# Kernel optimization log

Hardware: AMD Instinct MI355X
Metric: run time of the kernel (lower is better)

The kernel has to match this reference:

```python
import jax, jax.numpy as jnp
import numpy as np

B, T, D, U = 32, 2048, 512, 512


def setup_inputs() -> dict:
    key = jax.random.key(0)
    ks = jax.random.split(key, 6)
    scale = 0.05
    return {
        "values": jax.random.normal(ks[0], (B, T, D), dtype=jnp.float32),
        "query": jax.random.normal(ks[1], (B, D), dtype=jnp.float32),
        "W1_w": jax.random.normal(ks[2], (D, U), dtype=jnp.float32) * scale,
        "W1_b": jnp.zeros((U,), dtype=jnp.float32),
        "W2_w": jax.random.normal(ks[3], (D, U), dtype=jnp.float32) * scale,
        "W2_b": jnp.zeros((U,), dtype=jnp.float32),
        "V_w": jax.random.normal(ks[4], (U, 1), dtype=jnp.float32) * scale,
        "V_b": jnp.zeros((1,), dtype=jnp.float32),
    }


def reference(values, query, W1_w, W1_b, W2_w, W2_b, V_w, V_b):
    # values: [B, T, D]; query: [B, D]
    proj_v = jnp.einsum("btd,du->btu", values, W1_w) + W1_b          # [B, T, U]
    proj_q = (query @ W2_w + W2_b)[:, None, :]                        # [B, 1, U]
    score = jnp.tanh(proj_v + proj_q) @ V_w + V_b                     # [B, T, 1]
    attention_weights = jax.nn.softmax(score, axis=1)                 # [B, T, 1]
    context_vector = jnp.sum(attention_weights * values, axis=1)      # [B, D]
    return context_vector, attention_weights
```

## Files before the change

### kernel.cpp

```cpp
#include <hip/hip_runtime.h>
#include <hip/hip_bf16.h>
#include <stdint.h>


#define B_DIM 32
#define T_DIM 2048
#define D_DIM 512
#define U_DIM 512
#define M_DIM (B_DIM * T_DIM)

typedef short bf16x8 __attribute__((ext_vector_type(8)));
typedef float f32x4 __attribute__((ext_vector_type(4)));

__device__ __forceinline__ float fast_tanh(float x) {
    float e = __expf(2.0f * x);
    return 1.0f - __fdividef(2.0f, e + 1.0f);
}

__device__ __forceinline__ short bf16r(float x) {
    unsigned u = __float_as_uint(x);
    u += 0x7fffu + ((u >> 16) & 1u);
    return (short)(u >> 16);
}


__global__ void prep_kernel(const float* __restrict__ W1_w,
                            const float* __restrict__ W1_b,
                            const float* __restrict__ W2_w,
                            const float* __restrict__ W2_b,
                            const float* __restrict__ query,
                            unsigned short* __restrict__ W1T,
                            float* __restrict__ qb) {
    __shared__ float red[256];
    const int tid = threadIdx.x;
    if (blockIdx.x < 128) {
        int n = blockIdx.x * 256 + tid;
        int uu    = n & 255;
        int kc    = (n >> 8) & 3;
        int kstep = (n >> 10) & 15;
        int ut    = n >> 14;
        int u  = ut * 256 + uu;
        int k0 = kstep * 32 + kc * 8;
        bf16x8 pk;
#pragma unroll
        for (int j = 0; j < 8; ++j)
            pk[j] = bf16r(W1_w[(size_t)(k0 + j) * U_DIM + u]);
        ((bf16x8*)W1T)[n] = pk;
    } else {
        int bid = blockIdx.x - 128;
        int b  = bid >> 3;
        int ug = bid & 7;
        int u  = ug * 64 + (tid & 63);
        int dq = tid >> 6;
        const float* q  = query + b * D_DIM + dq * 128;
        const float* w2 = W2_w + (size_t)(dq * 128) * U_DIM + u;
        float acc = 0.f;
#pragma unroll 8
        for (int d = 0; d < 128; ++d)
            acc += q[d] * w2[(size_t)d * U_DIM];
        red[tid] = acc;
        __syncthreads();
        if (tid < 64) {
            qb[b * U_DIM + u] = red[tid] + red[tid + 64] + red[tid + 128]
                              + red[tid + 192] + W2_b[u] + W1_b[u];
        }
    }
}

__global__ __launch_bounds__(512, 4) void fused_kernel(
        const float* __restrict__ values,
        const unsigned short* __restrict__ W1T,
        const float* __restrict__ qb,
        const float* __restrict__ Vw,
        float* __restrict__ sP,
        float* __restrict__ Pms,
        float* __restrict__ Pctx) {
    __shared__ __align__(16) unsigned char Abuf[65536];
    __shared__ float sred[4][64];
    __shared__ float ew[64];
    __shared__ __align__(16) float red[4][512];

    const int tid  = threadIdx.x;
    const int lane = tid & 63;
    const int w    = tid >> 6;
    const int l15  = lane & 15;
    const int quad = lane >> 4;
    const int wr   = w >> 2;
    const int wc   = w & 3;
    const int chunk = blockIdx.x;
    const int mb   = chunk * 64;
    const int b    = mb >> 11;

    {
        const float* src = values + (size_t)mb * D_DIM;
#pragma unroll 8
        for (int it = 0; it < 16; ++it) {
            int idx = it * 2048 + tid * 4;
            f32x4 v = *(const f32x4*)(src + idx);
            int row = idx >> 9;
            int k   = idx & 511;
            union { __hip_bfloat162 h[2]; unsigned long long u; } pk;
            pk.h[0] = __float22bfloat162_rn(make_float2(v[0], v[1]));
            pk.h[1] = __float22bfloat162_rn(make_float2(v[2], v[3]));
            int addr = row * 1024 + ((((k >> 3) ^ (row & 7)) << 4) | ((k & 7) * 2));
            *(unsigned long long*)(Abuf + addr) = pk.u;
        }
    }
    __syncthreads();

    const unsigned short* bbase =
        W1T + ((size_t)(wc >> 1) * 16384 + quad * 256 + (wc & 1) * 128 + l15) * 8;
    const int r0 = wr * 32 + l15;
    const int r1 = r0 + 16;
    const int ksrot = chunk & 15;

    f32x4 acc[2][8] = {};

#pragma unroll 1
    for (int it = 0; it < 16; ++it) {
        const int ks = (it + ksrot) & 15;
        const unsigned short* bks = bbase + (size_t)ks * 8192;
        bf16x8 bfr[8];
#pragma unroll
        for (int ui = 0; ui < 8; ++ui)
            bfr[ui] = *(const bf16x8*)(bks + (size_t)ui * 128);

        const int slot = ks * 4 + quad;
        bf16x8 a0 = *(const bf16x8*)(Abuf + r0 * 1024 + ((slot ^ (r0 & 7)) << 4));
        bf16x8 a1 = *(const bf16x8*)(Abuf + r1 * 1024 + ((slot ^ (r1 & 7)) << 4));

        __builtin_amdgcn_sched_barrier(0);

        __builtin_amdgcn_s_setprio(1);
#pragma unroll
        for (int ui = 0; ui < 8; ++ui) {
            acc[0][ui] = __builtin_amdgcn_mfma_f32_16x16x32_bf16(a0, bfr[ui], acc[0][ui], 0, 0, 0);
            acc[1][ui] = __builtin_amdgcn_mfma_f32_16x16x32_bf16(a1, bfr[ui], acc[1][ui], 0, 0, 0);
        }
        __builtin_amdgcn_s_setprio(0);
        __builtin_amdgcn_sched_barrier(0);
    }

    const int ub = wc * 128 + l15;
    float sm[2][4] = {};
#pragma unroll
    for (int ui = 0; ui < 8; ++ui) {
        const int u = ub + ui * 16;
        const float qv = qb[b * U_DIM + u];
        const float vw = Vw[u];
#pragma unroll
        for (int mt = 0; mt < 2; ++mt)
#pragma unroll
            for (int r = 0; r < 4; ++r)
                sm[mt][r] += fast_tanh(acc[mt][ui][r] + qv) * vw;
    }
#pragma unroll
    for (int mt = 0; mt < 2; ++mt)
#pragma unroll
        for (int r = 0; r < 4; ++r) {
            float v = sm[mt][r];
            v += __shfl_xor(v, 1, 64);
            v += __shfl_xor(v, 2, 64);
            v += __shfl_xor(v, 4, 64);
            v += __shfl_xor(v, 8, 64);
            sm[mt][r] = v;
        }
    if (l15 == 0) {
#pragma unroll
        for (int mt = 0; mt < 2; ++mt)
#pragma unroll
            for (int r = 0; r < 4; ++r)
                sred[wc][wr * 32 + mt * 16 + quad * 4 + r] = sm[mt][r];
    }
    __syncthreads();

    if (tid < 64) {
        float s = sred[0][tid] + sred[1][tid] + sred[2][tid] + sred[3][tid];
        sP[mb + tid] = s;
        float m = s;
#pragma unroll
        for (int off = 1; off < 64; off <<= 1)
            m = fmaxf(m, __shfl_xor(m, off, 64));
        float e = __expf(s - m);
        ew[tid] = e;
        float S = e;
#pragma unroll
        for (int off = 1; off < 64; off <<= 1)
            S += __shfl_xor(S, off, 64);
        if (tid == 0) { Pms[chunk * 2] = m; Pms[chunk * 2 + 1] = S; }
    }
    __syncthreads();

    {
        const int d4 = tid & 127;
        const int th = tid >> 7;
        const float4* vb = (const float4*)(values + (size_t)(mb + th * 16) * D_DIM) + d4;
        float4 a = {0.f, 0.f, 0.f, 0.f};
#pragma unroll
        for (int i = 0; i < 16; ++i) {
            float e = ew[th * 16 + i];
            float4 v = vb[(size_t)i * 128];
            a.x += e * v.x; a.y += e * v.y;
            a.z += e * v.z; a.w += e * v.w;
        }
        ((float4*)red)[th * 128 + d4] = a;
    }
    __syncthreads();
    if (tid < 128) {
        float4 o0 = ((float4*)red)[tid];
        float4 o1 = ((float4*)red)[128 + tid];
        float4 o2 = ((float4*)red)[256 + tid];
        float4 o3 = ((float4*)red)[384 + tid];
        float4 o;
        o.x = o0.x + o1.x + o2.x + o3.x;
        o.y = o0.y + o1.y + o2.y + o3.y;
        o.z = o0.z + o1.z + o2.z + o3.z;
        o.w = o0.w + o1.w + o2.w + o3.w;
        *(float4*)(Pctx + (size_t)chunk * 512 + tid * 4) = o;
    }
}

__global__ void combine_kernel(const float* __restrict__ Pctx,
                               const float* __restrict__ Pms,
                               const float* __restrict__ sP,
                               float* __restrict__ out) {
    const int bid = blockIdx.x;
    const int b   = bid >> 3;
    const int p   = bid & 7;
    const int tid = threadIdx.x;

    float m = -1e30f;
#pragma unroll
    for (int c = 0; c < 32; ++c)
        m = fmaxf(m, Pms[(b * 32 + c) * 2]);
    float ec[32];
    float S = 0.f;
#pragma unroll
    for (int c = 0; c < 32; ++c) {
        ec[c] = __expf(Pms[(b * 32 + c) * 2] - m);
        S += ec[c] * Pms[(b * 32 + c) * 2 + 1];
    }
    const float invS = 1.0f / S;

    {
        const int d = p * 64 + tid;
        float a = 0.f;
#pragma unroll
        for (int c = 0; c < 32; ++c)
            a += ec[c] * Pctx[(size_t)(b * 32 + c) * 512 + d];
        out[b * D_DIM + d] = a * invS;
    }
#pragma unroll
    for (int j = 0; j < 4; ++j) {
        const int g = b * T_DIM + p * 256 + j * 64 + tid;
        out[B_DIM * D_DIM + g] = __expf(sP[g] - m) * invS;
    }
}

extern "C" void kernel_launch(void* const* d_in, const int* in_sizes, int n_in,
                              void* d_out, int out_size, void* d_ws, size_t ws_size,
                              hipStream_t stream) {
    const float* values = (const float*)d_in[0];
    const float* query  = (const float*)d_in[1];
    const float* W1_w   = (const float*)d_in[2];
    const float* W1_b   = (const float*)d_in[3];
    const float* W2_w   = (const float*)d_in[4];
    const float* W2_b   = (const float*)d_in[5];
    const float* V_w    = (const float*)d_in[6];

    float* out = (float*)d_out;

    unsigned char* ws = (unsigned char*)d_ws;
    unsigned short* W1T = (unsigned short*)(ws);
    float* qb  = (float*)(ws + 524288);
    float* sP  = (float*)(ws + 589824);
    float* Pms = (float*)(ws + 851968);
    float* Pctx= (float*)(ws + 860160);

    prep_kernel<<<384, 256, 0, stream>>>(W1_w, W1_b, W2_w, W2_b, query, W1T, qb);
    fused_kernel<<<1024, 512, 0, stream>>>(values, W1T, qb, V_w, sP, Pms, Pctx);
    combine_kernel<<<256, 64, 0, stream>>>(Pctx, Pms, sP, out);
}
```

Before: 264.6 us.

## Double tile rows per block and stage W1 slabs via async global-to-LDS loads

Each fused block now handles 128 rows instead of 64, so every W1 fragment feeds four MFMA row tiles instead of two and the grid shrinks to 512 blocks. W1 slabs are double-buffered in LDS with global_load_lds, and the values tile is converted to bf16 in four K-quarter stages. Softmax partials are reduced across two wavefronts, and the combine kernel now reads 16 chunks per batch. The aim is fewer global reads of W1 per row, at the cost of lower occupancy, more syncthreads per K step, and repeated A-staging stalls.

After: 260.1 us. About the same (-1.7%).

```diff
diff --git a/kernel.cpp b/kernel.cpp
--- a/kernel.cpp
+++ b/kernel.cpp
@@ -21,6 +21,14 @@
     unsigned u = __float_as_uint(x);
     u += 0x7fffu + ((u >> 16) & 1u);
     return (short)(u >> 16);
+}
+
+__device__ __forceinline__ void g2lds16(const void* g, void* lds) {
+    auto gp = reinterpret_cast<const __attribute__((address_space(1))) unsigned int*>(
+        reinterpret_cast<uintptr_t>(g));
+    auto lp = reinterpret_cast<__attribute__((address_space(3))) unsigned int*>(
+        (unsigned int)(uintptr_t)lds);
+    __builtin_amdgcn_global_load_lds(gp, lp, 16, 0, 0);
 }
 
 
@@ -67,7 +75,7 @@
     }
 }
 
-__global__ __launch_bounds__(512, 4) void fused_kernel(
+__global__ __launch_bounds__(512, 2) void fused_kernel(
         const float* __restrict__ values,
         const unsigned short* __restrict__ W1T,
         const float* __restrict__ qb,
@@ -75,9 +83,12 @@
         float* __restrict__ sP,
         float* __restrict__ Pms,
         float* __restrict__ Pctx) {
-    __shared__ __align__(16) unsigned char Abuf[65536];
-    __shared__ float sred[4][64];
-    __shared__ float ew[64];
+    __shared__ __align__(16) unsigned char Abuf[32768];
+    __shared__ __align__(16) unsigned char Bbuf[2][32768];
+    __shared__ float sred[4][128];
+    __shared__ float ew[128];
+    __shared__ float redm[2];
+    __shared__ float reds[2];
     __shared__ __align__(16) float red[4][512];
 
     const int tid  = threadIdx.x;
@@ -88,117 +99,155 @@
     const int wr   = w >> 2;
     const int wc   = w & 3;
     const int chunk = blockIdx.x;
-    const int mb   = chunk * 64;
+    const int mb   = chunk * 128;
     const int b    = mb >> 11;
 
-    {
-        const float* src = values + (size_t)mb * D_DIM;
-#pragma unroll 8
-        for (int it = 0; it < 16; ++it) {
+    const float* srcA = values + (size_t)mb * D_DIM;
+
+    auto stageA = [&](int q) {
+        f32x4 v[8];
+#pragma unroll
+        for (int it = 0; it < 8; ++it) {
             int idx = it * 2048 + tid * 4;
-            f32x4 v = *(const f32x4*)(src + idx);
-            int row = idx >> 9;
-            int k   = idx & 511;
+            int row = idx >> 7;
+            int kq  = idx & 127;
+            v[it] = *(const f32x4*)(srcA + (size_t)row * D_DIM + q * 128 + kq);
+        }
+#pragma unroll
+        for (int it = 0; it < 8; ++it) {
+            int idx = it * 2048 + tid * 4;
+            int row = idx >> 7;
+            int kq  = idx & 127;
             union { __hip_bfloat162 h[2]; unsigned long long u; } pk;
-            pk.h[0] = __float22bfloat162_rn(make_float2(v[0], v[1]));
-            pk.h[1] = __float22bfloat162_rn(make_float2(v[2], v[3]));
-            int addr = row * 1024 + ((((k >> 3) ^ (row & 7)) << 4) | ((k & 7) * 2));
+            pk.h[0] = __float22bfloat162_rn(make_float2(v[it][0], v[it][1]));
+            pk.h[1] = __float22bfloat162_rn(make_float2(v[it][2], v[it][3]));
+            int addr = row * 256 + ((((kq >> 3) ^ (row & 7)) << 4) | ((kq & 7) * 2));
             *(unsigned long long*)(Abuf + addr) = pk.u;
         }
-    }
-    __syncthreads();
-
-    const unsigned short* bbase =
-        W1T + ((size_t)(wc >> 1) * 16384 + quad * 256 + (wc & 1) * 128 + l15) * 8;
-    const int r0 = wr * 32 + l15;
-    const int r1 = r0 + 16;
-    const int ksrot = chunk & 15;
-
-    f32x4 acc[2][8] = {};
+    };
+    auto stageB = [&](int slab, int buf) {
+#pragma unroll
+        for (int i = 0; i < 4; ++i) {
+            int j = i * 512 + tid;
+            int ug = (j >> 10) * 16384 + slab * 1024 + (j & 1023);
+            g2lds16(W1T + (size_t)ug * 8, Bbuf[buf] + j * 16);
+        }
+    };
+
+    stageA(0);
+    stageB(0, 0);
+    __syncthreads();
+
+    const int bfo = (((wc >> 1) * 1024 + quad * 256 + (wc & 1) * 128 + l15) << 4);
+    const int ra[4] = { wr * 64 + l15,      wr * 64 + 16 + l15,
+                        wr * 64 + 32 + l15, wr * 64 + 48 + l15 };
+
+    f32x4 acc[4][8] = {};
+    int sel = 0;
 
 #pragma unroll 1
-    for (int it = 0; it < 16; ++it) {
-        const int ks = (it + ksrot) & 15;
-        const unsigned short* bks = bbase + (size_t)ks * 8192;
-        bf16x8 bfr[8];
-#pragma unroll
-        for (int ui = 0; ui < 8; ++ui)
-            bfr[ui] = *(const bf16x8*)(bks + (size_t)ui * 128);
-
-        const int slot = ks * 4 + quad;
-        bf16x8 a0 = *(const bf16x8*)(Abuf + r0 * 1024 + ((slot ^ (r0 & 7)) << 4));
-        bf16x8 a1 = *(const bf16x8*)(Abuf + r1 * 1024 + ((slot ^ (r1 & 7)) << 4));
-
-        __builtin_amdgcn_sched_barrier(0);
-
-        __builtin_amdgcn_s_setprio(1);
-#pragma unroll
-        for (int ui = 0; ui < 8; ++ui) {
-            acc[0][ui] = __builtin_amdgcn_mfma_f32_16x16x32_bf16(a0, bfr[ui], acc[0][ui], 0, 0, 0);
-            acc[1][ui] = __builtin_amdgcn_mfma_f32_16x16x32_bf16(a1, bfr[ui], acc[1][ui], 0, 0, 0);
-        }
-        __builtin_amdgcn_s_setprio(0);
-        __builtin_amdgcn_sched_barrier(0);
+    for (int q = 0; q < 4; ++q) {
+#pragma unroll 1
+        for (int s = 0; s < 4; ++s) {
+            const int slab = q * 4 + s;
+            if (slab < 15) stageB(slab + 1, sel ^ 1);
+
+            bf16x8 bfr[8];
+#pragma unroll
+            for (int ui = 0; ui < 8; ++ui)
+                bfr[ui] = *(const bf16x8*)(Bbuf[sel] + bfo + ui * 256);
+            const int slot = s * 4 + quad;
+            bf16x8 af[4];
+#pragma unroll
+            for (int mt = 0; mt < 4; ++mt)
+                af[mt] = *(const bf16x8*)(Abuf + ra[mt] * 256 + ((slot ^ (ra[mt] & 7)) << 4));
+
+            __builtin_amdgcn_sched_barrier(0);
+            __builtin_amdgcn_s_setprio(1);
+#pragma unroll
+            for (int ui = 0; ui < 8; ++ui) {
+#pragma unroll
+                for (int mt = 0; mt < 4; ++mt)
+                    acc[mt][ui] = __builtin_amdgcn_mfma_f32_16x16x32_bf16(
+                        af[mt], bfr[ui], acc[mt][ui], 0, 0, 0);
+            }
+            __builtin_amdgcn_s_setprio(0);
+            __builtin_amdgcn_sched_barrier(0);
+
+            __syncthreads();
+            sel ^= 1;
+        }
+        if (q < 3) {
+            stageA(q + 1);
+            __syncthreads();
+        }
     }
 
     const int ub = wc * 128 + l15;
-    float sm[2][4] = {};
+    float smv[4][4] = {};
 #pragma unroll
     for (int ui = 0; ui < 8; ++ui) {
         const int u = ub + ui * 16;
         const float qv = qb[b * U_DIM + u];
         const float vw = Vw[u];
 #pragma unroll
-        for (int mt = 0; mt < 2; ++mt)
+        for (int mt = 0; mt < 4; ++mt)
 #pragma unroll
             for (int r = 0; r < 4; ++r)
-                sm[mt][r] += fast_tanh(acc[mt][ui][r] + qv) * vw;
-    }
-#pragma unroll
-    for (int mt = 0; mt < 2; ++mt)
+                smv[mt][r] += fast_tanh(acc[mt][ui][r] + qv) * vw;
+    }
+#pragma unroll
+    for (int mt = 0; mt < 4; ++mt)
 #pragma unroll
         for (int r = 0; r < 4; ++r) {
-            float v = sm[mt][r];
+            float v = smv[mt][r];
             v += __shfl_xor(v, 1, 64);
             v += __shfl_xor(v, 2, 64);
             v += __shfl_xor(v, 4, 64);
             v += __shfl_xor(v, 8, 64);
-            sm[mt][r] = v;
+            smv[mt][r] = v;
         }
     if (l15 == 0) {
 #pragma unroll
-        for (int mt = 0; mt < 2; ++mt)
+        for (int mt = 0; mt < 4; ++mt)
 #pragma unroll
             for (int r = 0; r < 4; ++r)
-                sred[wc][wr * 32 + mt * 16 + quad * 4 + r] = sm[mt][r];
-    }
-    __syncthreads();
-
-    if (tid < 64) {
-        float s = sred[0][tid] + sred[1][tid] + sred[2][tid] + sred[3][tid];
+                sred[wc][wr * 64 + mt * 16 + quad * 4 + r] = smv[mt][r];
+    }
+    __syncthreads();
+
+    float s = 0.f;
+    if (tid < 128) {
+        s = sred[0][tid] + sred[1][tid] + sred[2][tid] + sred[3][tid];
         sP[mb + tid] = s;
         float m = s;
 #pragma unroll
         for (int off = 1; off < 64; off <<= 1)
             m = fmaxf(m, __shfl_xor(m, off, 64));
-        float e = __expf(s - m);
+        if ((tid & 63) == 0) redm[tid >> 6] = m;
+    }
+    __syncthreads();
+    const float mc = fmaxf(redm[0], redm[1]);
+    if (tid < 128) {
+        float e = __expf(s - mc);
         ew[tid] = e;
         float S = e;
 #pragma unroll
         for (int off = 1; off < 64; off <<= 1)
             S += __shfl_xor(S, off, 64);
-        if (tid == 0) { Pms[chunk * 2] = m; Pms[chunk * 2 + 1] = S; }
-    }
-    __syncthreads();
+        if ((tid & 63) == 0) reds[tid >> 6] = S;
+    }
+    __syncthreads();
+    if (tid == 0) { Pms[chunk * 2] = mc; Pms[chunk * 2 + 1] = reds[0] + reds[1]; }
 
     {
         const int d4 = tid & 127;
         const int th = tid >> 7;
-        const float4* vb = (const float4*)(values + (size_t)(mb + th * 16) * D_DIM) + d4;
+        const float4* vb = (const float4*)(values + (size_t)(mb + th * 32) * D_DIM) + d4;
         float4 a = {0.f, 0.f, 0.f, 0.f};
 #pragma unroll
-        for (int i = 0; i < 16; ++i) {
-            float e = ew[th * 16 + i];
+        for (int i = 0; i < 32; ++i) {
+            float e = ew[th * 32 + i];
             float4 v = vb[(size_t)i * 128];
             a.x += e * v.x; a.y += e * v.y;
             a.z += e * v.z; a.w += e * v.w;
@@ -231,14 +280,14 @@
 
     float m = -1e30f;
 #pragma unroll
-    for (int c = 0; c < 32; ++c)
-        m = fmaxf(m, Pms[(b * 32 + c) * 2]);
-    float ec[32];
+    for (int c = 0; c < 16; ++c)
+        m = fmaxf(m, Pms[(b * 16 + c) * 2]);
+    float ec[16];
     float S = 0.f;
 #pragma unroll
-    for (int c = 0; c < 32; ++c) {
-        ec[c] = __expf(Pms[(b * 32 + c) * 2] - m);
-        S += ec[c] * Pms[(b * 32 + c) * 2 + 1];
+    for (int c = 0; c < 16; ++c) {
+        ec[c] = __expf(Pms[(b * 16 + c) * 2] - m);
+        S += ec[c] * Pms[(b * 16 + c) * 2 + 1];
     }
     const float invS = 1.0f / S;
 
@@ -246,8 +295,8 @@
         const int d = p * 64 + tid;
         float a = 0.f;
 #pragma unroll
-        for (int c = 0; c < 32; ++c)
-            a += ec[c] * Pctx[(size_t)(b * 32 + c) * 512 + d];
+        for (int c = 0; c < 16; ++c)
+            a += ec[c] * Pctx[(size_t)(b * 16 + c) * 512 + d];
         out[b * D_DIM + d] = a * invS;
     }
 #pragma unroll
@@ -278,6 +327,6 @@
     float* Pctx= (float*)(ws + 860160);
 
     prep_kernel<<<384, 256, 0, stream>>>(W1_w, W1_b, W2_w, W2_b, query, W1T, qb);
-    fused_kernel<<<1024, 512, 0, stream>>>(values, W1T, qb, V_w, sP, Pms, Pctx);
+    fused_kernel<<<512, 512, 0, stream>>>(values, W1T, qb, V_w, sP, Pms, Pctx);
     combine_kernel<<<256, 64, 0, stream>>>(Pctx, Pms, sP, out);
 }
```
